# Kernel optimization log

Hardware: AMD Instinct MI355X
Metric: run time of the kernel (lower is better)

Reference implementation:

```python
import jax, jax.numpy as jnp
import numpy as np

D_MODEL = 1024
N_HEADS = 16
D_HEAD = D_MODEL // N_HEADS


def setup_inputs() -> dict:
    key = jax.random.key(0)
    k1, k2, k3 = jax.random.split(key, 3)
    B, T = 4, 2048
    x = jax.random.normal(k1, (B, T, D_MODEL), dtype=jnp.float32)
    # torch Linear(d, 3d, bias=False): y = x @ W.T ; we store W already transposed -> [d, 3d]
    w_qkv = jax.random.normal(k2, (D_MODEL, 3 * D_MODEL), dtype=jnp.float32) * (D_MODEL ** -0.5)
    w_proj = jax.random.normal(k3, (D_MODEL, D_MODEL), dtype=jnp.float32) * (D_MODEL ** -0.5)
    return {"x": x, "w_qkv": w_qkv, "w_proj": w_proj}


def reference(x, w_qkv, w_proj):
    B, T, C = x.shape
    H, Dh = N_HEADS, D_HEAD
    qkv = (x @ w_qkv).reshape(B, T, 3, H, Dh)
    q = jnp.transpose(qkv[:, :, 0], (0, 2, 1, 3))  # [B,H,T,Dh]
    k = jnp.transpose(qkv[:, :, 1], (0, 2, 1, 3))
    v = jnp.transpose(qkv[:, :, 2], (0, 2, 1, 3))
    scale = 1.0 / jnp.sqrt(jnp.asarray(Dh, dtype=x.dtype))
    att = jnp.einsum('bhqd,bhkd->bhqk', q, k) * scale  # [B,H,T,T]
    causal = jnp.tril(jnp.ones((T, T), dtype=bool))
    att = jnp.where(causal[None, None], att, jnp.asarray(-jnp.inf, dtype=att.dtype))
    att = jax.nn.softmax(att, axis=-1)
    y = jnp.einsum('bhqk,bhkd->bhqd', att, v)          # [B,H,T,Dh]
    y = jnp.transpose(y, (0, 2, 1, 3)).reshape(B, T, C)
    return y @ w_proj
```

## Files before the change

### kernel.cpp

```cpp
#include <hip/hip_runtime.h>
#include <hip/hip_bf16.h>
#include <cmath>

#define T_SEQ 2048
#define NHEADS 16
#define DHEAD 64
#define DMODEL 1024
#define CQKV 3072

typedef __attribute__((ext_vector_type(8))) short short8;
typedef __attribute__((ext_vector_type(8))) __bf16 bf16x8;
typedef __attribute__((ext_vector_type(4))) float floatx4;

#define LDS_CAST(p) ((__attribute__((address_space(3))) void*)(p))
#define GLB_CAST(p) ((const __attribute__((address_space(1))) void*)(p))

static __device__ __forceinline__ floatx4 mfma_bf16(short8 a, short8 b, floatx4 c) {
  return __builtin_amdgcn_mfma_f32_16x16x32_bf16(
      __builtin_bit_cast(bf16x8, a), __builtin_bit_cast(bf16x8, b), c, 0, 0, 0);
}

static __device__ __forceinline__ short f2bf(float f) {
  union { float f; unsigned u; } x; x.f = f;
  unsigned r = x.u + 0x7FFFu + ((x.u >> 16) & 1u);
  return (short)(r >> 16);
}

static __device__ __forceinline__ float bf2f(short s) {
  return __builtin_bit_cast(float, ((unsigned)(unsigned short)s) << 16);
}

static __device__ __forceinline__ float exp2_(float x) {
#if __has_builtin(__builtin_amdgcn_exp2f)
  return __builtin_amdgcn_exp2f(x);
#else
  return exp2f(x);
#endif
}

static __device__ __forceinline__ bool sniff_is_bf16(const unsigned* __restrict__ x) {
  int cnt = 0;
#pragma unroll
  for (int i = 0; i < 32; ++i) {
    unsigned e = (x[i] >> 7) & 0xFFu;
    cnt += (e >= 0x70u && e <= 0x8Fu) ? 1 : 0;
  }
  return cnt >= 16;
}

static __device__ __forceinline__ short8 load8f32(const char* p, size_t idx) {
  const float4* f = (const float4*)(p + idx * 4);
  float4 a = f[0], b = f[1];
  short8 r;
  r[0] = f2bf(a.x); r[1] = f2bf(a.y); r[2] = f2bf(a.z); r[3] = f2bf(a.w);
  r[4] = f2bf(b.x); r[5] = f2bf(b.y); r[6] = f2bf(b.z); r[7] = f2bf(b.w);
  return r;
}

__global__ __launch_bounds__(256) void prep(const char* __restrict__ x,
                                            short* __restrict__ xbf,
                                            const char* __restrict__ wqkv,
                                            short* __restrict__ wqkvT,
                                            const char* __restrict__ wproj,
                                            short* __restrict__ wprojT,
                                            const unsigned* __restrict__ xs) {
  const bool isbf = sniff_is_bf16(xs);
  const int bid = blockIdx.x;
  if (bid < 4096) {
    const int i = (bid * 256 + threadIdx.x) * 8;
    if (isbf) *(short8*)(xbf + i) = *(const short8*)((const short*)x + i);
    else      *(short8*)(xbf + i) = load8f32(x, (size_t)i);
    return;
  }
  __shared__ short tile[32][33];
  const char* w; short* wt; int N, bid2;
  if (bid < 4096 + 3072) { w = wqkv;  wt = wqkvT;  N = 3072; bid2 = bid - 4096; }
  else                   { w = wproj; wt = wprojT; N = 1024; bid2 = bid - 7168; }
  const int K = 1024;
  const int ntiles = N >> 5;
  const int n0 = (bid2 % ntiles) * 32, k0 = (bid2 / ntiles) * 32;
  const int tx = threadIdx.x & 31, ty = threadIdx.x >> 5;
#pragma unroll
  for (int i = 0; i < 4; ++i) {
    const int r = ty * 4 + i;
    const size_t off = (size_t)(k0 + r) * N + n0 + tx;
    tile[r][tx] = isbf ? ((const short*)w)[off] : f2bf(((const float*)w)[off]);
  }
  __syncthreads();
#pragma unroll
  for (int i = 0; i < 4; ++i) {
    const int r = ty * 4 + i;
    wt[(size_t)(n0 + r) * K + k0 + tx] = tile[tx][r];
  }
}

__global__ __launch_bounds__(256) void gemm128(const short* __restrict__ A,
                                               const short* __restrict__ Bt,
                                               void* __restrict__ C,
                                               short* __restrict__ C2,
                                               int M, int N, int K, int mode,
                                               const unsigned* __restrict__ xs) {
  const bool out_f32 = (mode == 1) ? !sniff_is_bf16(xs) : false;

  __shared__ short as[128 * 64];
  __shared__ short bs[128 * 64];
  const int tid = threadIdx.x;
  const int wid = tid >> 6, lane = tid & 63;
  const int quad = lane >> 4, l16 = lane & 15;
  const int wm = wid >> 1, wn = wid & 1;

  const int gx = (int)gridDim.x;
  const int nwg = gx * (int)gridDim.y;
  int bid = (int)blockIdx.y * gx + (int)blockIdx.x;
  bid = (bid & 7) * (nwg >> 3) + (bid >> 3);
  const int m0 = (bid / gx) * 128;
  const int n0 = (bid % gx) * 128;

  const int srl = lane >> 3;
  const int sch = ((lane & 7) ^ srl) * 8;

  const floatx4 zero4 = {0.f, 0.f, 0.f, 0.f};
  floatx4 acc[4][4];
#pragma unroll
  for (int i = 0; i < 4; ++i)
#pragma unroll
    for (int j = 0; j < 4; ++j) acc[i][j] = zero4;

  for (int kt = 0; kt < K; kt += 64) {
    __syncthreads();
#pragma unroll
    for (int i = 0; i < 4; ++i) {
      const int row = wid * 32 + i * 8;
      const short* ga = A + (size_t)(m0 + row + srl) * K + kt + sch;
      const short* gb = Bt + (size_t)(n0 + row + srl) * K + kt + sch;
      __builtin_amdgcn_global_load_lds(GLB_CAST(ga), LDS_CAST(as + row * 64), 16, 0, 0);
      __builtin_amdgcn_global_load_lds(GLB_CAST(gb), LDS_CAST(bs + row * 64), 16, 0, 0);
    }
    __syncthreads();

#pragma unroll
    for (int kc = 0; kc < 2; ++kc) {
      const int slot = ((kc * 4 + quad) ^ (l16 & 7)) * 8;
      short8 afr[4], bfr[4];
#pragma unroll
      for (int mt = 0; mt < 4; ++mt)
        afr[mt] = *(const short8*)&as[(wm * 64 + mt * 16 + l16) * 64 + slot];
#pragma unroll
      for (int nt = 0; nt < 4; ++nt)
        bfr[nt] = *(const short8*)&bs[(wn * 64 + nt * 16 + l16) * 64 + slot];
#pragma unroll
      for (int mt = 0; mt < 4; ++mt)
#pragma unroll
        for (int nt = 0; nt < 4; ++nt)
          acc[mt][nt] = mfma_bf16(afr[mt], bfr[nt], acc[mt][nt]);
    }
  }

  const int row0 = m0 + wm * 64 + quad * 4;
  const int col0 = n0 + wn * 64 + l16;
  if (mode == 2 && n0 >= 2048) {
#pragma unroll
    for (int mt = 0; mt < 4; ++mt)
#pragma unroll
      for (int nt = 0; nt < 4; ++nt)
#pragma unroll
        for (int r = 0; r < 4; ++r) {
          const int row = row0 + mt * 16 + r;
          const int col = col0 + nt * 16;
          const int d = col & 63, hh = (col >> 6) - 32;
          const int bb = row >> 11, t = row & 2047;
          C2[((size_t)(bb * 16 + hh) * 64 + d) * T_SEQ + t] = f2bf(acc[mt][nt][r]);
        }
  } else {
    const int outN = (mode == 2) ? 2048 : N;
#pragma unroll
    for (int mt = 0; mt < 4; ++mt)
#pragma unroll
      for (int nt = 0; nt < 4; ++nt)
#pragma unroll
        for (int r = 0; r < 4; ++r) {
          const size_t off = (size_t)(row0 + mt * 16 + r) * outN + col0 + nt * 16;
          if (out_f32) ((float*)C)[off] = acc[mt][nt][r];
          else         ((short*)C)[off] = f2bf(acc[mt][nt][r]);
        }
  }
}

__global__ __launch_bounds__(512) void attn(const short* __restrict__ qk,
                                            const short* __restrict__ vT,
                                            short* __restrict__ y) {
  __shared__ short ks[2][64 * 64];
  __shared__ short vs[2][64 * 64];
  __shared__ short ps[8][16][72];
  const int tid = threadIdx.x;
  const int wid = tid >> 6, lane = tid & 63;
  const int quad = lane >> 4, l16 = lane & 15;
  const int b = blockIdx.x >> 4, h = blockIdx.x & 15;
  const int q0 = ((int)gridDim.y - 1 - (int)blockIdx.y) * 128;
  const int qw0 = q0 + wid * 16;

  const short* qbase = qk + (size_t)b * T_SEQ * 2048 + h * DHEAD;
  const short* kbase = qbase + DMODEL;
  const short* vtb = vT + (size_t)(b * NHEADS + h) * DHEAD * T_SEQ;
  const float SC = 0.18033688011112042f;

  const int srl = lane >> 3;
  const int sch = ((lane & 7) ^ srl) * 8;

  short8 aq[2];
#pragma unroll
  for (int kc = 0; kc < 2; ++kc) {
    short8 raw = *(const short8*)(qbase + (size_t)(qw0 + l16) * 2048 + kc * 32 + quad * 8);
#pragma unroll
    for (int j = 0; j < 8; ++j) aq[kc][j] = f2bf(bf2f(raw[j]) * SC);
  }

  const floatx4 zero4 = {0.f, 0.f, 0.f, 0.f};
  floatx4 o[4], lacc = zero4;
#pragma unroll
  for (int i = 0; i < 4; ++i) o[i] = zero4;
  const short8 ones8 = {0x3F80, 0x3F80, 0x3F80, 0x3F80, 0x3F80, 0x3F80, 0x3F80, 0x3F80};

  const int kend = q0 + 128;

  {
    const int row = wid * 8 + srl;
    const short* gk = kbase + (size_t)row * 2048 + sch;
    const short* gv = vtb + (size_t)row * T_SEQ + sch;
    __builtin_amdgcn_global_load_lds(GLB_CAST(gk), LDS_CAST(&ks[0][(wid * 8) * 64]), 16, 0, 0);
    __builtin_amdgcn_global_load_lds(GLB_CAST(gv), LDS_CAST(&vs[0][(wid * 8) * 64]), 16, 0, 0);
  }

  int cur = 0;
  for (int kt = 0; kt < kend; kt += 64, cur ^= 1) {
    __syncthreads();

    {
      const int ktn = (kt + 64 < kend) ? kt + 64 : kt;
      const int nxt = cur ^ 1;
      const int row = wid * 8 + srl;
      const short* gk = kbase + (size_t)(ktn + row) * 2048 + sch;
      const short* gv = vtb + (size_t)row * T_SEQ + ktn + sch;
      __builtin_amdgcn_global_load_lds(GLB_CAST(gk), LDS_CAST(&ks[nxt][(wid * 8) * 64]), 16, 0, 0);
      __builtin_amdgcn_global_load_lds(GLB_CAST(gv), LDS_CAST(&vs[nxt][(wid * 8) * 64]), 16, 0, 0);
    }

    if (kt <= qw0 + 15) {
      const short* ksc = &ks[cur][0];
      const short* vsc = &vs[cur][0];

      floatx4 s[4];
#pragma unroll
      for (int nt = 0; nt < 4; ++nt) {
        s[nt] = zero4;
#pragma unroll
        for (int kc = 0; kc < 2; ++kc) {
          const int slot = ((kc * 4 + quad) ^ (l16 & 7)) * 8;
          const short8 bk = *(const short8*)&ksc[(nt * 16 + l16) * 64 + slot];
          s[nt] = mfma_bf16(aq[kc], bk, s[nt]);
        }
      }

      const bool full = (kt + 63 <= qw0);
#pragma unroll
      for (int nt = 0; nt < 4; ++nt)
#pragma unroll
        for (int r = 0; r < 4; ++r) {
          float p = exp2_(s[nt][r]);
          if (!full) {
            const int key = kt + nt * 16 + l16;
            const int q = qw0 + quad * 4 + r;
            p = (key <= q) ? p : 0.f;
          }
          s[nt][r] = p;
        }

#pragma unroll
      for (int nt = 0; nt < 4; ++nt)
#pragma unroll
        for (int r = 0; r < 4; ++r)
          ps[wid][quad * 4 + r][nt * 16 + l16] = f2bf(s[nt][r]);

#pragma unroll
      for (int kc = 0; kc < 2; ++kc) {
        const short8 ap = *(const short8*)&ps[wid][l16][kc * 32 + quad * 8];
        lacc = mfma_bf16(ap, ones8, lacc);
#pragma unroll
        for (int d4 = 0; d4 < 4; ++d4) {
          const int slot = ((kc * 4 + quad) ^ (l16 & 7)) * 8;
          const short8 bv = *(const short8*)&vsc[(d4 * 16 + l16) * 64 + slot];
          o[d4] = mfma_bf16(ap, bv, o[d4]);
        }
      }
    }
  }

  floatx4 inv;
#pragma unroll
  for (int r = 0; r < 4; ++r) inv[r] = 1.0f / lacc[r];
#pragma unroll
  for (int d4 = 0; d4 < 4; ++d4)
#pragma unroll
    for (int r = 0; r < 4; ++r) {
      const int q = qw0 + quad * 4 + r;
      y[(size_t)(b * T_SEQ + q) * DMODEL + h * DHEAD + d4 * 16 + l16] =
          f2bf(o[d4][r] * inv[r]);
    }
}

extern "C" void kernel_launch(void* const* d_in, const int* in_sizes, int n_in,
                              void* d_out, int out_size, void* d_ws, size_t ws_size,
                              hipStream_t stream) {
  const char* x = (const char*)d_in[0];
  const char* w_qkv = (const char*)d_in[1];
  const char* w_proj = (const char*)d_in[2];
  const unsigned* xs = (const unsigned*)d_in[0];

  short* qk = (short*)d_ws;
  short* vTb = qk + (size_t)8192 * 2048;
  short* wqkvT = vTb + (size_t)64 * 64 * 2048;
  short* wprojT = wqkvT + (size_t)3072 * 1024;
  short* xbf = wprojT + (size_t)1024 * 1024;
  short* ybuf = xbf;

  prep<<<4096 + 3072 + 1024, 256, 0, stream>>>(x, xbf, w_qkv, wqkvT, w_proj, wprojT, xs);
  {
    dim3 grid(3072 / 128, 8192 / 128);
    gemm128<<<grid, 256, 0, stream>>>(xbf, wqkvT, qk, vTb, 8192, 3072, 1024, 2, xs);
  }
  {
    dim3 grid(4 * NHEADS, T_SEQ / 128);
    attn<<<grid, 512, 0, stream>>>(qk, vTb, ybuf);
  }
  {
    dim3 grid(1024 / 128, 8192 / 128);
    gemm128<<<grid, 256, 0, stream>>>(ybuf, wprojT, d_out, nullptr, 8192, 1024, 1024, 1, xs);
  }
}
```

Before: 253.3 us.

## Process two 128-row query sub-tiles per attention block to reuse K/V tiles

Each attention workgroup now covers 256 query rows as two 128-row sub-tiles sharing the same K/V LDS tiles, halving the grid along the sequence axis. This halves redundant K/V global-to-LDS loading per head. Query scaling moves from a pre-scale of Q into the exp2 argument, which adds a multiply per score element. Costs are more accumulator registers and fewer blocks (512), which may reduce occupancy and worsen causal load balance because block work is more uneven.

Measured after the change: 265.1 us. 4.7% more time.

```diff
diff --git a/kernel.cpp b/kernel.cpp
--- a/kernel.cpp
+++ b/kernel.cpp
@@ -196,32 +196,35 @@
   const int wid = tid >> 6, lane = tid & 63;
   const int quad = lane >> 4, l16 = lane & 15;
   const int b = blockIdx.x >> 4, h = blockIdx.x & 15;
-  const int q0 = ((int)gridDim.y - 1 - (int)blockIdx.y) * 128;
-  const int qw0 = q0 + wid * 16;
+  const int q0 = ((int)gridDim.y - 1 - (int)blockIdx.y) * 256;
 
   const short* qbase = qk + (size_t)b * T_SEQ * 2048 + h * DHEAD;
   const short* kbase = qbase + DMODEL;
   const short* vtb = vT + (size_t)(b * NHEADS + h) * DHEAD * T_SEQ;
-  const float SC = 0.18033688011112042f;
+  const float SCL = 0.18033688011112042f;
 
   const int srl = lane >> 3;
   const int sch = ((lane & 7) ^ srl) * 8;
 
-  short8 aq[2];
-#pragma unroll
-  for (int kc = 0; kc < 2; ++kc) {
-    short8 raw = *(const short8*)(qbase + (size_t)(qw0 + l16) * 2048 + kc * 32 + quad * 8);
-#pragma unroll
-    for (int j = 0; j < 8; ++j) aq[kc][j] = f2bf(bf2f(raw[j]) * SC);
-  }
+  short8 aq[2][2];
+#pragma unroll
+  for (int sub = 0; sub < 2; ++sub)
+#pragma unroll
+    for (int kc = 0; kc < 2; ++kc)
+      aq[sub][kc] = *(const short8*)(qbase +
+          (size_t)(q0 + sub * 128 + wid * 16 + l16) * 2048 + kc * 32 + quad * 8);
 
   const floatx4 zero4 = {0.f, 0.f, 0.f, 0.f};
-  floatx4 o[4], lacc = zero4;
-#pragma unroll
-  for (int i = 0; i < 4; ++i) o[i] = zero4;
+  floatx4 o[2][4], lacc[2];
+#pragma unroll
+  for (int sub = 0; sub < 2; ++sub) {
+    lacc[sub] = zero4;
+#pragma unroll
+    for (int i = 0; i < 4; ++i) o[sub][i] = zero4;
+  }
   const short8 ones8 = {0x3F80, 0x3F80, 0x3F80, 0x3F80, 0x3F80, 0x3F80, 0x3F80, 0x3F80};
 
-  const int kend = q0 + 128;
+  const int kend = q0 + 256;
 
   {
     const int row = wid * 8 + srl;
@@ -245,9 +248,13 @@
       __builtin_amdgcn_global_load_lds(GLB_CAST(gv), LDS_CAST(&vs[nxt][(wid * 8) * 64]), 16, 0, 0);
     }
 
-    if (kt <= qw0 + 15) {
-      const short* ksc = &ks[cur][0];
-      const short* vsc = &vs[cur][0];
+    const short* ksc = &ks[cur][0];
+    const short* vsc = &vs[cur][0];
+
+#pragma unroll
+    for (int sub = 0; sub < 2; ++sub) {
+      const int qw0 = q0 + sub * 128 + wid * 16;
+      if (kt > qw0 + 15) continue;
 
       floatx4 s[4];
 #pragma unroll
@@ -257,7 +264,7 @@
         for (int kc = 0; kc < 2; ++kc) {
           const int slot = ((kc * 4 + quad) ^ (l16 & 7)) * 8;
           const short8 bk = *(const short8*)&ksc[(nt * 16 + l16) * 64 + slot];
-          s[nt] = mfma_bf16(aq[kc], bk, s[nt]);
+          s[nt] = mfma_bf16(aq[sub][kc], bk, s[nt]);
         }
       }
 
@@ -266,7 +273,7 @@
       for (int nt = 0; nt < 4; ++nt)
 #pragma unroll
         for (int r = 0; r < 4; ++r) {
-          float p = exp2_(s[nt][r]);
+          float p = exp2_(s[nt][r] * SCL);
           if (!full) {
             const int key = kt + nt * 16 + l16;
             const int q = qw0 + quad * 4 + r;
@@ -284,28 +291,31 @@
 #pragma unroll
       for (int kc = 0; kc < 2; ++kc) {
         const short8 ap = *(const short8*)&ps[wid][l16][kc * 32 + quad * 8];
-        lacc = mfma_bf16(ap, ones8, lacc);
+        lacc[sub] = mfma_bf16(ap, ones8, lacc[sub]);
 #pragma unroll
         for (int d4 = 0; d4 < 4; ++d4) {
           const int slot = ((kc * 4 + quad) ^ (l16 & 7)) * 8;
           const short8 bv = *(const short8*)&vsc[(d4 * 16 + l16) * 64 + slot];
-          o[d4] = mfma_bf16(ap, bv, o[d4]);
+          o[sub][d4] = mfma_bf16(ap, bv, o[sub][d4]);
         }
       }
     }
   }
 
-  floatx4 inv;
-#pragma unroll
-  for (int r = 0; r < 4; ++r) inv[r] = 1.0f / lacc[r];
-#pragma unroll
-  for (int d4 = 0; d4 < 4; ++d4)
-#pragma unroll
-    for (int r = 0; r < 4; ++r) {
-      const int q = qw0 + quad * 4 + r;
-      y[(size_t)(b * T_SEQ + q) * DMODEL + h * DHEAD + d4 * 16 + l16] =
-          f2bf(o[d4][r] * inv[r]);
-    }
+#pragma unroll
+  for (int sub = 0; sub < 2; ++sub) {
+    floatx4 inv;
+#pragma unroll
+    for (int r = 0; r < 4; ++r) inv[r] = 1.0f / lacc[sub][r];
+#pragma unroll
+    for (int d4 = 0; d4 < 4; ++d4)
+#pragma unroll
+      for (int r = 0; r < 4; ++r) {
+        const int q = q0 + sub * 128 + wid * 16 + quad * 4 + r;
+        y[(size_t)(b * T_SEQ + q) * DMODEL + h * DHEAD + d4 * 16 + l16] =
+            f2bf(o[sub][d4][r] * inv[r]);
+      }
+  }
 }
 
 extern "C" void kernel_launch(void* const* d_in, const int* in_sizes, int n_in,
@@ -329,7 +339,7 @@
     gemm128<<<grid, 256, 0, stream>>>(xbf, wqkvT, qk, vTb, 8192, 3072, 1024, 2, xs);
   }
   {
-    dim3 grid(4 * NHEADS, T_SEQ / 128);
+    dim3 grid(4 * NHEADS, T_SEQ / 256);
     attn<<<grid, 512, 0, stream>>>(qk, vTb, ybuf);
   }
   {
```
